# Kernel optimization log

Hardware: AMD Instinct MI355X
Metric: run time of the kernel (lower is better)

Reference implementation:

```python
import jax, jax.numpy as jnp
import numpy as np

N_NODES = 100000
N_EDGES = 3200000
D_IN = 256
D_OUT = 256


def setup_inputs() -> dict:
    key = jax.random.key(0)
    k1, k2, k3, k4, k5 = jax.random.split(key, 5)
    x = jax.random.normal(k1, (N_NODES, D_IN), dtype=jnp.float32)
    weight = jax.random.normal(k2, (D_IN, D_OUT), dtype=jnp.float32) * (1.0 / np.sqrt(D_IN))
    edge_row = jax.random.randint(k3, (N_EDGES,), 0, N_NODES, dtype=jnp.int32)
    edge_col = jax.random.randint(k4, (N_EDGES,), 0, N_NODES, dtype=jnp.int32)
    edge_val = jax.random.uniform(k5, (N_EDGES,), dtype=jnp.float32)
    return {"x": x, "weight": weight, "edge_row": edge_row,
            "edge_col": edge_col, "edge_val": edge_val}


def reference(x, weight, edge_row, edge_col, edge_val):
    # support = dropout(x) @ W  (dropout p=0 -> identity, eval-mode math)
    support = x @ weight                       # [N, D_OUT]
    # output = spmm(adj, support): for each edge (r, c, v): out[r] += v * support[c]
    gathered = edge_val[:, None] * support[edge_col]   # [E, D_OUT]
    output = jax.ops.segment_sum(gathered, edge_row, num_segments=N_NODES)
    return output
```

## Files before the change

kernel.cpp:

```cpp
#include <hip/hip_runtime.h>

#define N_NODES 100000
#define N_EDGES 3200000
#define DIM 256

typedef _Float16 half_t;
typedef __attribute__((ext_vector_type(4))) _Float16 half4;
typedef __attribute__((ext_vector_type(8))) _Float16 half8;
typedef __attribute__((ext_vector_type(4))) float floatx4;

__global__ __launch_bounds__(256) void castw_kernel(const float* __restrict__ w,
                                                    half_t* __restrict__ wT) {
    __shared__ float tile[32][33];
    int bk = blockIdx.x * 32;
    int bn = blockIdx.y * 32;
    int tx = threadIdx.x & 31, ty = threadIdx.x >> 5;
#pragma unroll
    for (int i = 0; i < 4; i++)
        tile[ty + i * 8][tx] = w[(size_t)(bk + ty + i * 8) * DIM + bn + tx];
    __syncthreads();
#pragma unroll
    for (int i = 0; i < 4; i++)
        wT[(size_t)(bn + ty + i * 8) * DIM + bk + tx] = (half_t)tile[tx][ty + i * 8];
}

#define BM 128
#define BK 32
#define LDK 40

__global__ __launch_bounds__(512) void gemm_f16_kernel(const float* __restrict__ A,
                                                       const half_t* __restrict__ BT,
                                                       half_t* __restrict__ C, int M) {
    __shared__ half_t As[BM][LDK];
    __shared__ half_t Bs[256][LDK];

    const int tid = threadIdx.x;
    const int wid = tid >> 6, lane = tid & 63;
    const int wm = wid & 1, wn = wid >> 1;
    const int row0 = blockIdx.x * BM;
    const int lr = lane & 15;
    const int quad = lane >> 4;

    floatx4 acc[4][4] = {};

    const int ar = tid >> 2;
    const int ac = (tid & 3) * 8;
    const bool avalid = (row0 + ar) < M;
    const float* aptr = A + (size_t)(row0 + ar) * DIM + ac;

    for (int k0 = 0; k0 < DIM; k0 += BK) {
        {
            const float4* src = (const float4*)(aptr + k0);
            half_t* dst = &As[ar][ac];
#pragma unroll
            for (int i = 0; i < 2; i++) {
                float4 v = avalid ? src[i] : make_float4(0.f, 0.f, 0.f, 0.f);
                half4 h;
                h.x = (half_t)v.x; h.y = (half_t)v.y;
                h.z = (half_t)v.z; h.w = (half_t)v.w;
                ((half4*)dst)[i] = h;
            }
        }
        {
#pragma unroll
            for (int i = 0; i < 2; i++) {
                int ch = tid + i * 512;
                int r = ch >> 2, cb = (ch & 3) * 8;
                half8 v = *(const half8*)(BT + (size_t)r * DIM + k0 + cb);
                *(half8*)&Bs[r][cb] = v;
            }
        }
        __syncthreads();

        half8 a[4], b[4];
#pragma unroll
        for (int i = 0; i < 4; i++)
            a[i] = *(const half8*)&As[wm * 64 + i * 16 + lr][quad * 8];
#pragma unroll
        for (int j = 0; j < 4; j++)
            b[j] = *(const half8*)&Bs[wn * 64 + j * 16 + lr][quad * 8];
#pragma unroll
        for (int i = 0; i < 4; i++)
#pragma unroll
            for (int j = 0; j < 4; j++)
                acc[i][j] = __builtin_amdgcn_mfma_f32_16x16x32_f16(a[i], b[j], acc[i][j], 0, 0, 0);
        __syncthreads();
    }

#pragma unroll
    for (int i = 0; i < 4; i++) {
#pragma unroll
        for (int j = 0; j < 4; j++) {
            int gc = wn * 64 + j * 16 + lr;
            int grb = row0 + wm * 64 + i * 16 + quad * 4;
#pragma unroll
            for (int r = 0; r < 4; r++) {
                int gr = grb + r;
                if (gr < M) C[(size_t)gr * DIM + gc] = (half_t)acc[i][j][r];
            }
        }
    }
}

#define NBUCK 391
#define EPB 16384
#define NEB ((N_EDGES + EPB - 1) / EPB)

__global__ __launch_bounds__(256) void bucket_hist_kernel(const int* __restrict__ erow,
                                                          int* __restrict__ bcnt) {
    __shared__ int lh[NBUCK];
    for (int b = threadIdx.x; b < NBUCK; b += 256) lh[b] = 0;
    __syncthreads();
    int base4 = blockIdx.x * (EPB / 4);
#pragma unroll
    for (int i = 0; i < 16; i++) {
        int idx4 = base4 + i * 256 + threadIdx.x;
        if (idx4 < N_EDGES / 4) {
            int4 r4 = ((const int4*)erow)[idx4];
            atomicAdd(&lh[r4.x >> 8], 1);
            atomicAdd(&lh[r4.y >> 8], 1);
            atomicAdd(&lh[r4.z >> 8], 1);
            atomicAdd(&lh[r4.w >> 8], 1);
        }
    }
    __syncthreads();
    for (int b = threadIdx.x; b < NBUCK; b += 256)
        if (lh[b]) atomicAdd(&bcnt[b * 16], lh[b]);
}

__global__ __launch_bounds__(512) void scan_buckets_kernel(int* __restrict__ bcnt,
                                                           int* __restrict__ bbase,
                                                           int* __restrict__ offsets) {
    __shared__ int s[512];
    int t = threadIdx.x;
    int v = (t < NBUCK) ? bcnt[t * 16] : 0;
    s[t] = v;
    __syncthreads();
    for (int off = 1; off < 512; off <<= 1) {
        int u = (t >= off) ? s[t - off] : 0;
        __syncthreads();
        s[t] += u;
        __syncthreads();
    }
    if (t < NBUCK) {
        int ex = s[t] - v;
        bbase[t] = ex;
        bcnt[t * 16] = ex;
    }
    if (t == 0) { bbase[NBUCK] = N_EDGES; offsets[N_NODES] = N_EDGES; }
}

__global__ __launch_bounds__(256) void bucket_scatter_kernel(const int* __restrict__ erow,
                                                             const int* __restrict__ ecol,
                                                             const float* __restrict__ eval,
                                                             int* __restrict__ bcursor,
                                                             int2* __restrict__ tmp) {
    __shared__ int lh[NBUCK];
    __shared__ int lbase[NBUCK];
    for (int b = threadIdx.x; b < NBUCK; b += 256) lh[b] = 0;
    __syncthreads();

    int base4 = blockIdx.x * (EPB / 4);
#pragma unroll
    for (int i = 0; i < 16; i++) {
        int idx4 = base4 + i * 256 + threadIdx.x;
        if (idx4 < N_EDGES / 4) {
            int4 r4 = ((const int4*)erow)[idx4];
            atomicAdd(&lh[r4.x >> 8], 1);
            atomicAdd(&lh[r4.y >> 8], 1);
            atomicAdd(&lh[r4.z >> 8], 1);
            atomicAdd(&lh[r4.w >> 8], 1);
        }
    }
    __syncthreads();
    for (int b = threadIdx.x; b < NBUCK; b += 256) {
        int c = lh[b];
        lbase[b] = c ? atomicAdd(&bcursor[b * 16], c) : 0;
        lh[b] = 0;
    }
    __syncthreads();

#define SCAT(R, C, V)                                                     \
    {                                                                     \
        int _r = (R), _c = (C);                                           \
        int _b = _r >> 8;                                                 \
        int _rank = atomicAdd(&lh[_b], 1);                                \
        tmp[lbase[_b] + _rank] =                                          \
            make_int2(((_r & 255) << 17) | _c, __float_as_int(V));        \
    }
#pragma unroll
    for (int i = 0; i < 16; i++) {
        int idx4 = base4 + i * 256 + threadIdx.x;
        if (idx4 < N_EDGES / 4) {
            int4 r4 = ((const int4*)erow)[idx4];
            int4 c4 = ((const int4*)ecol)[idx4];
            float4 v4 = ((const float4*)eval)[idx4];
            SCAT(r4.x, c4.x, v4.x);
            SCAT(r4.y, c4.y, v4.y);
            SCAT(r4.z, c4.z, v4.z);
            SCAT(r4.w, c4.w, v4.w);
        }
    }
#undef SCAT
}

__global__ __launch_bounds__(256) void bucket_to_csr_kernel(const int2* __restrict__ tmp,
                                                            const int* __restrict__ bbase,
                                                            int* __restrict__ offsets,
                                                            int2* __restrict__ sedge) {
    __shared__ int lh[256];
    __shared__ int s[256];
    const int b = blockIdx.x;
    const int t = threadIdx.x;
    const int beg = bbase[b], end = bbase[b + 1];

    lh[t] = 0;
    __syncthreads();
    for (int e = beg + t; e < end; e += 256)
        atomicAdd(&lh[tmp[e].x >> 17], 1);
    __syncthreads();

    int c = lh[t];
    s[t] = c;
    __syncthreads();
    for (int off = 1; off < 256; off <<= 1) {
        int u = (t >= off) ? s[t - off] : 0;
        __syncthreads();
        s[t] += u;
        __syncthreads();
    }
    int ex = s[t] - c;
    int row = (b << 8) + t;
    if (row < N_NODES) offsets[row] = beg + ex;
    lh[t] = ex;
    __syncthreads();

    for (int e = beg + t; e < end; e += 256) {
        int2 q = tmp[e];
        int lr = q.x >> 17;
        int rank = atomicAdd(&lh[lr], 1);
        sedge[beg + rank] = make_int2(q.x & 0x1FFFF, q.y);
    }
}

__global__ __launch_bounds__(256) void spmm_kernel(const half_t* __restrict__ support,
                                                   const int* __restrict__ offsets,
                                                   const int2* __restrict__ edges,
                                                   float* __restrict__ out) {
    int row = (blockIdx.x * blockDim.x + threadIdx.x) >> 6;
    if (row >= N_NODES) return;
    int lane = threadIdx.x & 63;
    int h = lane >> 5;
    int j = lane & 31;

    int beg = offsets[row];
    int end = offsets[row + 1];

    float acc[8] = {0.f, 0.f, 0.f, 0.f, 0.f, 0.f, 0.f, 0.f};
    int e = beg;

    if ((e & 1) && e < end) {
        int2 q0 = edges[e];
        half8 s0 = *(const half8*)(support + (size_t)q0.x * DIM + j * 8);
        float v0 = (h == 0) ? __int_as_float(q0.y) : 0.f;
#pragma unroll
        for (int d = 0; d < 8; d++) acc[d] += v0 * (float)s0[d];
        e++;
    }

    for (; e + 15 < end; e += 16) {
        int4 pa = *(const int4*)(edges + e + 2 * h);
        int4 pb = *(const int4*)(edges + e + 4 + 2 * h);
        int4 pc = *(const int4*)(edges + e + 8 + 2 * h);
        int4 pd = *(const int4*)(edges + e + 12 + 2 * h);
        half8 s0 = *(const half8*)(support + (size_t)pa.x * DIM + j * 8);
        half8 s1 = *(const half8*)(support + (size_t)pa.z * DIM + j * 8);
        half8 s2 = *(const half8*)(support + (size_t)pb.x * DIM + j * 8);
        half8 s3 = *(const half8*)(support + (size_t)pb.z * DIM + j * 8);
        half8 s4 = *(const half8*)(support + (size_t)pc.x * DIM + j * 8);
        half8 s5 = *(const half8*)(support + (size_t)pc.z * DIM + j * 8);
        half8 s6 = *(const half8*)(support + (size_t)pd.x * DIM + j * 8);
        half8 s7 = *(const half8*)(support + (size_t)pd.z * DIM + j * 8);
        float v0 = __int_as_float(pa.y), v1 = __int_as_float(pa.w);
        float v2 = __int_as_float(pb.y), v3 = __int_as_float(pb.w);
        float v4 = __int_as_float(pc.y), v5 = __int_as_float(pc.w);
        float v6 = __int_as_float(pd.y), v7 = __int_as_float(pd.w);
#pragma unroll
        for (int d = 0; d < 8; d++)
            acc[d] += v0 * (float)s0[d] + v1 * (float)s1[d]
                    + v2 * (float)s2[d] + v3 * (float)s3[d]
                    + v4 * (float)s4[d] + v5 * (float)s5[d]
                    + v6 * (float)s6[d] + v7 * (float)s7[d];
    }
    for (; e + 1 < end; e += 2) {
        int2 q0 = edges[e + h];
        half8 s0 = *(const half8*)(support + (size_t)q0.x * DIM + j * 8);
        float v0 = __int_as_float(q0.y);
#pragma unroll
        for (int d = 0; d < 8; d++) acc[d] += v0 * (float)s0[d];
    }
    if (e < end) {
        int2 q0 = edges[e];
        half8 s0 = *(const half8*)(support + (size_t)q0.x * DIM + j * 8);
        float v0 = (h == 0) ? __int_as_float(q0.y) : 0.f;
#pragma unroll
        for (int d = 0; d < 8; d++) acc[d] += v0 * (float)s0[d];
    }

    float r0, r1, r2, r3, g0, g1, g2, g3;
    if (h == 0) {
        r0 = acc[0]; r1 = acc[1]; r2 = acc[2]; r3 = acc[3];
        g0 = acc[4]; g1 = acc[5]; g2 = acc[6]; g3 = acc[7];
    } else {
        r0 = acc[4]; r1 = acc[5]; r2 = acc[6]; r3 = acc[7];
        g0 = acc[0]; g1 = acc[1]; g2 = acc[2]; g3 = acc[3];
    }
    r0 += __shfl_xor(g0, 32, 64);
    r1 += __shfl_xor(g1, 32, 64);
    r2 += __shfl_xor(g2, 32, 64);
    r3 += __shfl_xor(g3, 32, 64);

    *(float4*)(out + (size_t)row * DIM + j * 8 + h * 4) = make_float4(r0, r1, r2, r3);
}

extern "C" void kernel_launch(void* const* d_in, const int* in_sizes, int n_in,
                              void* d_out, int out_size, void* d_ws, size_t ws_size,
                              hipStream_t stream) {
    const float* x    = (const float*)d_in[0];
    const float* w    = (const float*)d_in[1];
    const int*   erow = (const int*)d_in[2];
    const int*   ecol = (const int*)d_in[3];
    const float* eval = (const float*)d_in[4];
    float* out = (float*)d_out;

    char* ws = (char*)d_ws;
    half_t* support = (half_t*)ws;
    int*    offsets = (int*)(ws + 51200000);
    int2*   sedge   = (int2*)(ws + 51600128);
    half_t* wT      = (half_t*)(ws + 77200128);
    int*    bcnt    = (int*)(ws + 77331200);
    int*    bbase   = (int*)(ws + 77356224);
    int2*   tmp     = (int2*)d_out;

    hipMemsetAsync(bcnt, 0, NBUCK * 16 * sizeof(int), stream);

    castw_kernel<<<dim3(8, 8), 256, 0, stream>>>(w, wT);

    dim3 ggrid((N_NODES + BM - 1) / BM, 1);
    gemm_f16_kernel<<<ggrid, 512, 0, stream>>>(x, wT, support, N_NODES);

    bucket_hist_kernel<<<NEB, 256, 0, stream>>>(erow, bcnt);
    scan_buckets_kernel<<<1, 512, 0, stream>>>(bcnt, bbase, offsets);
    bucket_scatter_kernel<<<NEB, 256, 0, stream>>>(erow, ecol, eval, bcnt, tmp);
    bucket_to_csr_kernel<<<NBUCK, 256, 0, stream>>>(tmp, bbase, offsets, sedge);

    spmm_kernel<<<(N_NODES * 64 + 255) / 256, 256, 0, stream>>>(support, offsets,
                                                                sedge, out);
}
```

Before: 544.4 us.

## Drop bucket histogram pass using fixed-capacity buckets; add nontemporal loads/stores

Removes the separate histogram kernel. The scatter kernel now writes each bucket into a fixed-capacity slot (CAP entries per bucket) inside the temporary buffer, and the bucket counts are scanned afterwards to place edges into the final CSR. This saves one full pass over the edge row array and one kernel launch. It relies on no bucket exceeding CAP edges (expected count about 8200 for uniform inputs) and on tmp (391*16384*8 bytes) fitting in the output buffer. It also adds nontemporal loads and stores in the GEMM, scatter and SpMM kernels, reduces edges per block, and sets an occupancy hint on the SpMM kernel.

```diff
diff --git a/kernel.cpp b/kernel.cpp
--- a/kernel.cpp
+++ b/kernel.cpp
@@ -8,6 +8,7 @@
 typedef __attribute__((ext_vector_type(4))) _Float16 half4;
 typedef __attribute__((ext_vector_type(8))) _Float16 half8;
 typedef __attribute__((ext_vector_type(4))) float floatx4;
+typedef __attribute__((ext_vector_type(4))) int intx4;
 
 __global__ __launch_bounds__(256) void castw_kernel(const float* __restrict__ w,
                                                     half_t* __restrict__ wT) {
@@ -50,11 +51,12 @@
 
     for (int k0 = 0; k0 < DIM; k0 += BK) {
         {
-            const float4* src = (const float4*)(aptr + k0);
+            const floatx4* src = (const floatx4*)(aptr + k0);
             half_t* dst = &As[ar][ac];
 #pragma unroll
             for (int i = 0; i < 2; i++) {
-                float4 v = avalid ? src[i] : make_float4(0.f, 0.f, 0.f, 0.f);
+                floatx4 v = avalid ? __builtin_nontemporal_load(src + i)
+                                   : (floatx4){0.f, 0.f, 0.f, 0.f};
                 half4 h;
                 h.x = (half_t)v.x; h.y = (half_t)v.y;
                 h.z = (half_t)v.z; h.w = (half_t)v.w;
@@ -103,52 +105,9 @@
 }
 
 #define NBUCK 391
-#define EPB 16384
+#define CAP 16384
+#define EPB 4096
 #define NEB ((N_EDGES + EPB - 1) / EPB)
-
-__global__ __launch_bounds__(256) void bucket_hist_kernel(const int* __restrict__ erow,
-                                                          int* __restrict__ bcnt) {
-    __shared__ int lh[NBUCK];
-    for (int b = threadIdx.x; b < NBUCK; b += 256) lh[b] = 0;
-    __syncthreads();
-    int base4 = blockIdx.x * (EPB / 4);
-#pragma unroll
-    for (int i = 0; i < 16; i++) {
-        int idx4 = base4 + i * 256 + threadIdx.x;
-        if (idx4 < N_EDGES / 4) {
-            int4 r4 = ((const int4*)erow)[idx4];
-            atomicAdd(&lh[r4.x >> 8], 1);
-            atomicAdd(&lh[r4.y >> 8], 1);
-            atomicAdd(&lh[r4.z >> 8], 1);
-            atomicAdd(&lh[r4.w >> 8], 1);
-        }
-    }
-    __syncthreads();
-    for (int b = threadIdx.x; b < NBUCK; b += 256)
-        if (lh[b]) atomicAdd(&bcnt[b * 16], lh[b]);
-}
-
-__global__ __launch_bounds__(512) void scan_buckets_kernel(int* __restrict__ bcnt,
-                                                           int* __restrict__ bbase,
-                                                           int* __restrict__ offsets) {
-    __shared__ int s[512];
-    int t = threadIdx.x;
-    int v = (t < NBUCK) ? bcnt[t * 16] : 0;
-    s[t] = v;
-    __syncthreads();
-    for (int off = 1; off < 512; off <<= 1) {
-        int u = (t >= off) ? s[t - off] : 0;
-        __syncthreads();
-        s[t] += u;
-        __syncthreads();
-    }
-    if (t < NBUCK) {
-        int ex = s[t] - v;
-        bbase[t] = ex;
-        bcnt[t * 16] = ex;
-    }
-    if (t == 0) { bbase[NBUCK] = N_EDGES; offsets[N_NODES] = N_EDGES; }
-}
 
 __global__ __launch_bounds__(256) void bucket_scatter_kernel(const int* __restrict__ erow,
                                                              const int* __restrict__ ecol,
@@ -162,10 +121,10 @@
 
     int base4 = blockIdx.x * (EPB / 4);
 #pragma unroll
-    for (int i = 0; i < 16; i++) {
+    for (int i = 0; i < 4; i++) {
         int idx4 = base4 + i * 256 + threadIdx.x;
         if (idx4 < N_EDGES / 4) {
-            int4 r4 = ((const int4*)erow)[idx4];
+            intx4 r4 = __builtin_nontemporal_load((const intx4*)erow + idx4);
             atomicAdd(&lh[r4.x >> 8], 1);
             atomicAdd(&lh[r4.y >> 8], 1);
             atomicAdd(&lh[r4.z >> 8], 1);
@@ -175,7 +134,7 @@
     __syncthreads();
     for (int b = threadIdx.x; b < NBUCK; b += 256) {
         int c = lh[b];
-        lbase[b] = c ? atomicAdd(&bcursor[b * 16], c) : 0;
+        lbase[b] = c ? (b * CAP + atomicAdd(&bcursor[b * 16], c)) : 0;
         lh[b] = 0;
     }
     __syncthreads();
@@ -189,12 +148,12 @@
             make_int2(((_r & 255) << 17) | _c, __float_as_int(V));        \
     }
 #pragma unroll
-    for (int i = 0; i < 16; i++) {
+    for (int i = 0; i < 4; i++) {
         int idx4 = base4 + i * 256 + threadIdx.x;
         if (idx4 < N_EDGES / 4) {
-            int4 r4 = ((const int4*)erow)[idx4];
-            int4 c4 = ((const int4*)ecol)[idx4];
-            float4 v4 = ((const float4*)eval)[idx4];
+            intx4 r4 = __builtin_nontemporal_load((const intx4*)erow + idx4);
+            intx4 c4 = __builtin_nontemporal_load((const intx4*)ecol + idx4);
+            floatx4 v4 = __builtin_nontemporal_load((const floatx4*)eval + idx4);
             SCAT(r4.x, c4.x, v4.x);
             SCAT(r4.y, c4.y, v4.y);
             SCAT(r4.z, c4.z, v4.z);
@@ -204,7 +163,26 @@
 #undef SCAT
 }
 
+__global__ __launch_bounds__(512) void scan_buckets_kernel(const int* __restrict__ bcnt,
+                                                           int* __restrict__ bbase,
+                                                           int* __restrict__ offsets) {
+    __shared__ int s[512];
+    int t = threadIdx.x;
+    int v = (t < NBUCK) ? bcnt[t * 16] : 0;
+    s[t] = v;
+    __syncthreads();
+    for (int off = 1; off < 512; off <<= 1) {
+        int u = (t >= off) ? s[t - off] : 0;
+        __syncthreads();
+        s[t] += u;
+        __syncthreads();
+    }
+    if (t < NBUCK) bbase[t] = s[t] - v;
+    if (t == 0) { bbase[NBUCK] = N_EDGES; offsets[N_NODES] = N_EDGES; }
+}
+
 __global__ __launch_bounds__(256) void bucket_to_csr_kernel(const int2* __restrict__ tmp,
+                                                            const int* __restrict__ bcnt,
                                                             const int* __restrict__ bbase,
                                                             int* __restrict__ offsets,
                                                             int2* __restrict__ sedge) {
@@ -212,12 +190,14 @@
     __shared__ int s[256];
     const int b = blockIdx.x;
     const int t = threadIdx.x;
-    const int beg = bbase[b], end = bbase[b + 1];
+    const int cnt = bcnt[b * 16];
+    const int obase = bbase[b];
+    const int2* src = tmp + (size_t)b * CAP;
 
     lh[t] = 0;
     __syncthreads();
-    for (int e = beg + t; e < end; e += 256)
-        atomicAdd(&lh[tmp[e].x >> 17], 1);
+    for (int e = t; e < cnt; e += 256)
+        atomicAdd(&lh[src[e].x >> 17], 1);
     __syncthreads();
 
     int c = lh[t];
@@ -231,22 +211,22 @@
     }
     int ex = s[t] - c;
     int row = (b << 8) + t;
-    if (row < N_NODES) offsets[row] = beg + ex;
+    if (row < N_NODES) offsets[row] = obase + ex;
     lh[t] = ex;
     __syncthreads();
 
-    for (int e = beg + t; e < end; e += 256) {
-        int2 q = tmp[e];
+    for (int e = t; e < cnt; e += 256) {
+        int2 q = src[e];
         int lr = q.x >> 17;
         int rank = atomicAdd(&lh[lr], 1);
-        sedge[beg + rank] = make_int2(q.x & 0x1FFFF, q.y);
-    }
-}
-
-__global__ __launch_bounds__(256) void spmm_kernel(const half_t* __restrict__ support,
-                                                   const int* __restrict__ offsets,
-                                                   const int2* __restrict__ edges,
-                                                   float* __restrict__ out) {
+        sedge[obase + rank] = make_int2(q.x & 0x1FFFF, q.y);
+    }
+}
+
+__global__ __launch_bounds__(256, 8) void spmm_kernel(const half_t* __restrict__ support,
+                                                      const int* __restrict__ offsets,
+                                                      const int2* __restrict__ edges,
+                                                      float* __restrict__ out) {
     int row = (blockIdx.x * blockDim.x + threadIdx.x) >> 6;
     if (row >= N_NODES) return;
     int lane = threadIdx.x & 63;
@@ -269,10 +249,10 @@
     }
 
     for (; e + 15 < end; e += 16) {
-        int4 pa = *(const int4*)(edges + e + 2 * h);
-        int4 pb = *(const int4*)(edges + e + 4 + 2 * h);
-        int4 pc = *(const int4*)(edges + e + 8 + 2 * h);
-        int4 pd = *(const int4*)(edges + e + 12 + 2 * h);
+        intx4 pa = __builtin_nontemporal_load((const intx4*)(edges + e + 2 * h));
+        intx4 pb = __builtin_nontemporal_load((const intx4*)(edges + e + 4 + 2 * h));
+        intx4 pc = __builtin_nontemporal_load((const intx4*)(edges + e + 8 + 2 * h));
+        intx4 pd = __builtin_nontemporal_load((const intx4*)(edges + e + 12 + 2 * h));
         half8 s0 = *(const half8*)(support + (size_t)pa.x * DIM + j * 8);
         half8 s1 = *(const half8*)(support + (size_t)pa.z * DIM + j * 8);
         half8 s2 = *(const half8*)(support + (size_t)pb.x * DIM + j * 8);
@@ -320,7 +300,8 @@
     r2 += __shfl_xor(g2, 32, 64);
     r3 += __shfl_xor(g3, 32, 64);
 
-    *(float4*)(out + (size_t)row * DIM + j * 8 + h * 4) = make_float4(r0, r1, r2, r3);
+    floatx4 res = {r0, r1, r2, r3};
+    __builtin_nontemporal_store(res, (floatx4*)(out + (size_t)row * DIM + j * 8 + h * 4));
 }
 
 extern "C" void kernel_launch(void* const* d_in, const int* in_sizes, int n_in,
@@ -349,10 +330,9 @@
     dim3 ggrid((N_NODES + BM - 1) / BM, 1);
     gemm_f16_kernel<<<ggrid, 512, 0, stream>>>(x, wT, support, N_NODES);
 
-    bucket_hist_kernel<<<NEB, 256, 0, stream>>>(erow, bcnt);
+    bucket_scatter_kernel<<<NEB, 256, 0, stream>>>(erow, ecol, eval, bcnt, tmp);
     scan_buckets_kernel<<<1, 512, 0, stream>>>(bcnt, bbase, offsets);
-    bucket_scatter_kernel<<<NEB, 256, 0, stream>>>(erow, ecol, eval, bcnt, tmp);
-    bucket_to_csr_kernel<<<NBUCK, 256, 0, stream>>>(tmp, bbase, offsets, sedge);
+    bucket_to_csr_kernel<<<NBUCK, 256, 0, stream>>>(tmp, bcnt, bbase, offsets, sedge);
 
     spmm_kernel<<<(N_NODES * 64 + 255) / 256, 256, 0, stream>>>(support, offsets,
                                                                 sedge, out);
```

After: 611.4 us. 12.3% more time.
